# Optimization experiments

Hardware: AMD Instinct MI355X
Metric: run time of the kernel (lower is better)

## Reference

```python
import jax, jax.numpy as jnp
import numpy as np

T, B, IN, H, F, OUT = 2048, 32, 256, 512, 2048, 256


def setup_inputs() -> dict:
    key = jax.random.key(0)
    ks = jax.random.split(key, 9)
    s_in = 1.0 / np.sqrt(IN)
    s_h = 1.0 / np.sqrt(H)
    s_f = 1.0 / np.sqrt(F)
    return {
        "x": jax.random.normal(ks[0], (T, B, IN), dtype=jnp.float32),
        "Wg": jax.random.uniform(ks[1], (H, IN), jnp.float32, -s_in, s_in),
        "bg": jax.random.uniform(ks[2], (H,), jnp.float32, -s_in, s_in),
        "Wi": jax.random.uniform(ks[3], (H, IN), jnp.float32, -s_in, s_in),
        "bi": jax.random.uniform(ks[4], (H,), jnp.float32, -s_in, s_in),
        "W1": jax.random.uniform(ks[5], (F, H), jnp.float32, -s_h, s_h),
        "b1": jax.random.uniform(ks[6], (F,), jnp.float32, -s_h, s_h),
        "W2": jax.random.uniform(ks[7], (OUT, F), jnp.float32, -s_f, s_f),
        "b2": jax.random.uniform(ks[8], (OUT,), jnp.float32, -s_f, s_f),
    }


def _gilr_scan(a, b):
    # h_t = a_t * h_{t-1} + b_t with h_0 = 0  ->  parallel associative scan over time
    def combine(c1, c2):
        a1, b1 = c1
        a2, b2 = c2
        return (a1 * a2, b1 * a2 + b2)
    _, h = jax.lax.associative_scan(combine, (a, b), axis=0)
    return h


def reference(x, Wg, bg, Wi, bi, W1, b1, W2, b2):
    # x: (T, B, IN)
    g = jax.nn.sigmoid(jnp.einsum("tbi,hi->tbh", x, Wg) + bg)  # (T,B,H)
    i = jnp.tanh(jnp.einsum("tbi,hi->tbh", x, Wi) + bi)        # (T,B,H)
    h = _gilr_scan(g, (1.0 - g) * i)                             # (T,B,H)
    z = jax.nn.gelu(jnp.einsum("tbh,fh->tbf", h, W1) + b1, approximate=False)
    out = jnp.einsum("tbf,of->tbo", z, W2) + b2                  # (T,B,OUT)
    return out
```

## Files before the change

kernel.cpp:

```cpp
#include <hip/hip_runtime.h>
#include <hip/hip_fp16.h>
#include <math.h>


#define IN_DIM 256
#define H_DIM 512
#define F_DIM 2048
#define OUT_DIM 256

typedef _Float16 f16;
typedef _Float16 f16x8 __attribute__((ext_vector_type(8)));
typedef float f32x4 __attribute__((ext_vector_type(4)));

#define AS3(p) ((__attribute__((address_space(3))) void*)(p))
#define AS1(p) ((const __attribute__((address_space(1))) void*)(p))
#define MFMA16(d, x, y) d = __builtin_amdgcn_mfma_f32_16x16x32_f16(x, y, d, 0, 0, 0)


__global__ void cvt_kernel(const float* __restrict__ in, f16* __restrict__ out, int n8) {
  int i = blockIdx.x * blockDim.x + threadIdx.x;
  if (i >= n8) return;
  const float4* p = (const float4*)in + (size_t)i * 2;
  float4 a = p[0], b = p[1];
  f16x8 o = { (f16)a.x, (f16)a.y, (f16)a.z, (f16)a.w,
              (f16)b.x, (f16)b.y, (f16)b.z, (f16)b.w };
  *((f16x8*)out + i) = o;
}

__global__ void bias_cat_kernel(const float* __restrict__ bg, const float* __restrict__ bi,
                                float* __restrict__ bgi) {
  int t = threadIdx.x;
  bgi[t] = (t < 512) ? bg[t] : bi[t - 512];
}

__device__ __forceinline__ float sigmoid_fast(float v) {
  return __builtin_amdgcn_rcpf(1.0f + __expf(-v));
}
__device__ __forceinline__ float tanh_fast(float v) {
  return 1.0f - 2.0f * __builtin_amdgcn_rcpf(__expf(2.0f * v) + 1.0f);
}
__device__ __forceinline__ float gelu_fast(float v) {
  float u = v * v;
  float y = v * fmaf(0.0713548353f, u, 1.59576912161f);
  return v * __builtin_amdgcn_rcpf(1.0f + __expf(-y));
}


__global__ __launch_bounds__(256, 4) void gemm1_k(
    const f16* __restrict__ A, const f16* __restrict__ Bw,
    const float* __restrict__ bias, f16* __restrict__ Cout) {
  constexpr int LDA = 256, LDB = 256, LDC = 1024, NT = 8;
  __shared__ f16 lds[2][2][128][32];
  const int tid = threadIdx.x, wid = tid >> 6, lane = tid & 63;
  const int bid = blockIdx.x;
  const int m0 = ((bid & 7) * 64 + (bid >> 6)) * 128;
  const int n0 = ((bid >> 3) & 7) * 128;
  const int wr = (wid >> 1) * 64, wc = (wid & 1) * 64;

  const f16* srcA[2]; const f16* srcB[2];
#pragma unroll
  for (int q = 0; q < 2; ++q) {
    int s = (wid * 2 + q) * 64 + lane;
    int row = s >> 2, g = (s & 3) ^ ((row >> 1) & 3);
    srcA[q] = A + (size_t)(m0 + row) * LDA + g * 8;
    srcB[q] = Bw + (size_t)(n0 + row) * LDB + g * 8;
  }
  auto stage = [&](int buf, int kt) {
    f16* la = &lds[buf][0][0][0] + (wid * 2) * 512;
    f16* lb = &lds[buf][1][0][0] + (wid * 2) * 512;
#pragma unroll
    for (int q = 0; q < 2; ++q) {
      __builtin_amdgcn_global_load_lds(AS1(srcA[q] + kt * 32), AS3(la + q * 512), 16, 0, 0);
      __builtin_amdgcn_global_load_lds(AS1(srcB[q] + kt * 32), AS3(lb + q * 512), 16, 0, 0);
    }
  };
  const int r = lane & 15;
  const int cs = (((lane >> 4) ^ ((lane >> 1) & 3)) << 3);

  f32x4 acc[4][4] = {};
  stage(0, 0);
  for (int kt = 0; kt < NT; ++kt) {
    __syncthreads();
    if (kt + 1 < NT) stage((kt + 1) & 1, kt + 1);
    f16(*At)[32] = lds[kt & 1][0];
    f16(*Bt)[32] = lds[kt & 1][1];
    f16x8 af[4], bf[4];
#pragma unroll
    for (int i = 0; i < 4; ++i) af[i] = *(const f16x8*)&At[wr + i * 16 + r][cs];
#pragma unroll
    for (int i = 0; i < 4; ++i) bf[i] = *(const f16x8*)&Bt[wc + i * 16 + r][cs];
#pragma unroll
    for (int mi = 0; mi < 4; ++mi)
#pragma unroll
      for (int ni = 0; ni < 4; ++ni)
        MFMA16(acc[mi][ni], af[mi], bf[ni]);
  }

  __syncthreads();
  const bool sig = n0 < 512;
  f16* ep = &lds[0][0][0][0] + wid * 4096;
  const int rq = (lane >> 4) * 4;
#pragma unroll
  for (int ni = 0; ni < 4; ++ni) {
    float bv = bias[n0 + wc + ni * 16 + r];
    int cc = ni * 2 + (r >> 3);
#pragma unroll
    for (int mi = 0; mi < 4; ++mi) {
#pragma unroll
      for (int j = 0; j < 4; ++j) {
        int lrow = mi * 16 + rq + j;
        float v = acc[mi][ni][j] + bv;
        float av = sig ? sigmoid_fast(v) : tanh_fast(v);
        ep[lrow * 64 + ((cc ^ (lrow & 7)) << 3) + (r & 7)] = (f16)av;
      }
    }
  }
  asm volatile("s_waitcnt lgkmcnt(0)" ::: "memory");
  __builtin_amdgcn_sched_barrier(0);
#pragma unroll
  for (int t = 0; t < 8; ++t) {
    int idx = t * 64 + lane;
    int row = idx >> 3, c = idx & 7;
    f16x8 v = *(const f16x8*)(ep + row * 64 + ((c ^ (row & 7)) << 3));
    *(f16x8*)(Cout + (size_t)(m0 + wr + row) * LDC + n0 + wc + c * 8) = v;
  }
}


__global__ __launch_bounds__(256, 4) void gemm2_k(
    const f16* __restrict__ A, const f16* __restrict__ Bw,
    const float* __restrict__ bias, f16* __restrict__ Cout) {
  constexpr int LDA = 1024, LDB = 512, LDC = 2048, NT = 16;
  __shared__ f16 lds[2][2][128][32];
  const int tid = threadIdx.x, wid = tid >> 6, lane = tid & 63;
  const int bid = blockIdx.x;
  const int m0 = ((bid & 7) * 16 + (bid >> 7)) * 128;
  const int n0 = ((bid >> 3) & 15) * 128;
  const int wr = (wid >> 1) * 64, wc = (wid & 1) * 64;

  const f16* srcA[2]; const f16* srcB[2];
#pragma unroll
  for (int q = 0; q < 2; ++q) {
    int s = (wid * 2 + q) * 64 + lane;
    int row = s >> 2, g = (s & 3) ^ ((row >> 1) & 3);
    srcA[q] = A + (size_t)(m0 + row) * LDA + g * 8;
    srcB[q] = Bw + (size_t)(n0 + row) * LDB + g * 8;
  }
  auto stage = [&](int buf, int kt) {
    f16* la = &lds[buf][0][0][0] + (wid * 2) * 512;
    f16* lb = &lds[buf][1][0][0] + (wid * 2) * 512;
#pragma unroll
    for (int q = 0; q < 2; ++q) {
      __builtin_amdgcn_global_load_lds(AS1(srcA[q] + kt * 32), AS3(la + q * 512), 16, 0, 0);
      __builtin_amdgcn_global_load_lds(AS1(srcB[q] + kt * 32), AS3(lb + q * 512), 16, 0, 0);
    }
  };
  const int r = lane & 15;
  const int cs = (((lane >> 4) ^ ((lane >> 1) & 3)) << 3);

  f32x4 acc[4][4] = {};
  stage(0, 0);
  for (int kt = 0; kt < NT; ++kt) {
    __syncthreads();
    if (kt + 1 < NT) stage((kt + 1) & 1, kt + 1);
    f16(*At)[32] = lds[kt & 1][0];
    f16(*Bt)[32] = lds[kt & 1][1];
    f16x8 af[4], bf[4];
#pragma unroll
    for (int i = 0; i < 4; ++i) af[i] = *(const f16x8*)&At[wr + i * 16 + r][cs];
#pragma unroll
    for (int i = 0; i < 4; ++i) bf[i] = *(const f16x8*)&Bt[wc + i * 16 + r][cs];
#pragma unroll
    for (int mi = 0; mi < 4; ++mi)
#pragma unroll
      for (int ni = 0; ni < 4; ++ni)
        MFMA16(acc[mi][ni], af[mi], bf[ni]);
  }

  __syncthreads();
  f16* ep = &lds[0][0][0][0] + wid * 4096;
  const int rq = (lane >> 4) * 4;
#pragma unroll
  for (int ni = 0; ni < 4; ++ni) {
    float bv = bias[n0 + wc + ni * 16 + r];
    int cc = ni * 2 + (r >> 3);
#pragma unroll
    for (int mi = 0; mi < 4; ++mi) {
#pragma unroll
      for (int j = 0; j < 4; ++j) {
        int lrow = mi * 16 + rq + j;
        float v = gelu_fast(acc[mi][ni][j] + bv);
        ep[lrow * 64 + ((cc ^ (lrow & 7)) << 3) + (r & 7)] = (f16)v;
      }
    }
  }
  asm volatile("s_waitcnt lgkmcnt(0)" ::: "memory");
  __builtin_amdgcn_sched_barrier(0);
#pragma unroll
  for (int t = 0; t < 8; ++t) {
    int idx = t * 64 + lane;
    int row = idx >> 3, c = idx & 7;
    f16x8 v = *(const f16x8*)(ep + row * 64 + ((c ^ (row & 7)) << 3));
    *(f16x8*)(Cout + (size_t)(m0 + wr + row) * LDC + n0 + wc + c * 8) = v;
  }
}


__global__ __launch_bounds__(256, 2) void gemm3_k(
    const f16* __restrict__ A, const f16* __restrict__ Bw,
    const float* __restrict__ bias, float* __restrict__ Cout) {
  constexpr int LDA = 2048, LDB = 2048, LDC = 256, NT = 32;
  __shared__ f16 lds[2][2][128][64];
  const int tid = threadIdx.x, wid = tid >> 6, lane = tid & 63;
  const int bid = blockIdx.x;
  const int m0 = ((bid & 7) * 16 + (bid >> 4)) * 128;
  const int n0 = ((bid >> 3) & 1) * 128;
  const int wr = (wid >> 1) * 64, wc = (wid & 1) * 64;

  auto stage = [&](int buf, int kt) {
    const f16* ga = A + (size_t)m0 * LDA + kt * 64;
    const f16* gb = Bw + (size_t)n0 * LDB + kt * 64;
    f16* la = &lds[buf][0][0][0];
    f16* lb = &lds[buf][1][0][0];
#pragma unroll
    for (int q = 0; q < 4; ++q) {
      int seg = (wid << 2) + q;
      int s = seg * 64 + lane;
      int row = s >> 3, col = (s & 7) << 3;
      __builtin_amdgcn_global_load_lds(AS1(ga + (size_t)row * LDA + col),
                                       AS3(la + seg * 512), 16, 0, 0);
      __builtin_amdgcn_global_load_lds(AS1(gb + (size_t)row * LDB + col),
                                       AS3(lb + seg * 512), 16, 0, 0);
    }
  };

  f32x4 acc[4][4] = {};
  stage(0, 0);
  for (int kt = 0; kt < NT; ++kt) {
    __syncthreads();
    if (kt + 1 < NT) stage((kt + 1) & 1, kt + 1);
    f16(*At)[64] = lds[kt & 1][0];
    f16(*Bt)[64] = lds[kt & 1][1];
    const int r = lane & 15, cg = (lane >> 4) << 3;
#pragma unroll
    for (int kk = 0; kk < 2; ++kk) {
      f16x8 af[4], bf[4];
#pragma unroll
      for (int i = 0; i < 4; ++i)
        af[i] = *(const f16x8*)&At[wr + i * 16 + r][kk * 32 + cg];
#pragma unroll
      for (int i = 0; i < 4; ++i)
        bf[i] = *(const f16x8*)&Bt[wc + i * 16 + r][kk * 32 + cg];
#pragma unroll
      for (int mi = 0; mi < 4; ++mi)
#pragma unroll
        for (int ni = 0; ni < 4; ++ni)
          MFMA16(acc[mi][ni], af[mi], bf[ni]);
    }
  }
  const int r = lane & 15, rq = (lane >> 4) * 4;
#pragma unroll
  for (int ni = 0; ni < 4; ++ni) {
    int col = n0 + wc + ni * 16 + r;
    float bv = bias[col];
#pragma unroll
    for (int mi = 0; mi < 4; ++mi) {
#pragma unroll
      for (int j = 0; j < 4; ++j) {
        int row = m0 + wr + mi * 16 + rq + j;
        Cout[(size_t)row * LDC + col] = acc[mi][ni][j] + bv;
      }
    }
  }
}


#define NCH 16384
#define NCHUNK 32
#define CLEN 64

__global__ void scan_p1(const f16* __restrict__ ab, float* __restrict__ cA,
                        float* __restrict__ cH) {
  int ch = blockIdx.x * 256 + threadIdx.x;
  int c = blockIdx.y;
  const f16* pg = ab + (size_t)(c * CLEN) * 32768 + (ch >> 9) * 1024 + (ch & 511);
  const f16* pi = pg + 512;
  float A = 1.f, Hl = 0.f;
  for (int t = 0; t < CLEN; ++t) {
    float g = (float)pg[0];
    float ii = (float)pi[0];
    Hl = fmaf(g, Hl - ii, ii);
    A *= g;
    pg += 32768; pi += 32768;
  }
  cA[c * NCH + ch] = A;
  cH[c * NCH + ch] = Hl;
}

__global__ void scan_p2(const float* __restrict__ cA, const float* __restrict__ cH,
                        float* __restrict__ st) {
  int ch = blockIdx.x * 256 + threadIdx.x;
  float h0 = 0.f;
  for (int c = 0; c < NCHUNK; ++c) {
    st[c * NCH + ch] = h0;
    h0 = cA[c * NCH + ch] * h0 + cH[c * NCH + ch];
  }
}

__global__ void scan_p3(f16* __restrict__ ab, const float* __restrict__ st) {
  int ch = blockIdx.x * 256 + threadIdx.x;
  int c = blockIdx.y;
  f16* pg = ab + (size_t)(c * CLEN) * 32768 + (ch >> 9) * 1024 + (ch & 511);
  const f16* pi = pg + 512;
  float hv = st[c * NCH + ch];
  for (int t = 0; t < CLEN; ++t) {
    float g = (float)pg[0];
    float ii = (float)pi[0];
    hv = fmaf(g, hv - ii, ii);
    pg[0] = (f16)hv;
    pg += 32768; pi += 32768;
  }
}


extern "C" void kernel_launch(void* const* d_in, const int* in_sizes, int n_in,
                              void* d_out, int out_size, void* d_ws, size_t ws_size,
                              hipStream_t stream) {
  const float* x  = (const float*)d_in[0];
  const float* Wg = (const float*)d_in[1];
  const float* bg = (const float*)d_in[2];
  const float* Wi = (const float*)d_in[3];
  const float* bi = (const float*)d_in[4];
  const float* W1 = (const float*)d_in[5];
  const float* b1 = (const float*)d_in[6];
  const float* W2 = (const float*)d_in[7];
  const float* b2 = (const float*)d_in[8];
  float* out = (float*)d_out;

  char* ws = (char*)d_ws;
  f16*   wgi16 = (f16*)(ws + 0);
  f16*   w116  = (f16*)(ws + 524288);
  f16*   w216  = (f16*)(ws + 2621440);
  float* bgi   = (float*)(ws + 3670016);
  f16*   x16   = (f16*)(ws + 4194304);
  f16*   ab16  = (f16*)(ws + 37748736);
  float* cA    = (float*)(ws + 171966464);
  float* cH    = (float*)(ws + 174063616);
  float* st    = (float*)(ws + 176160768);
  f16*   z16   = (f16*)(ws + 178257920);
  if (ws_size < 245366784) return;

  cvt_kernel<<<64, 256, 0, stream>>>(Wg, wgi16, 16384);
  cvt_kernel<<<64, 256, 0, stream>>>(Wi, wgi16 + 131072, 16384);
  cvt_kernel<<<512, 256, 0, stream>>>(W1, w116, 131072);
  cvt_kernel<<<256, 256, 0, stream>>>(W2, w216, 65536);
  bias_cat_kernel<<<1, 1024, 0, stream>>>(bg, bi, bgi);
  cvt_kernel<<<8192, 256, 0, stream>>>(x, x16, 2097152);

  gemm1_k<<<4096, 256, 0, stream>>>(x16, wgi16, bgi, ab16);

  scan_p1<<<dim3(64, NCHUNK), 256, 0, stream>>>(ab16, cA, cH);
  scan_p2<<<64, 256, 0, stream>>>(cA, cH, st);
  scan_p3<<<dim3(64, NCHUNK), 256, 0, stream>>>(ab16, st);

  for (int s = 0; s < 4; ++s) {
    const f16* hs = ab16 + (size_t)s * 16384 * 1024;
    gemm2_k<<<2048, 256, 0, stream>>>(hs, w116, b1, z16);
    gemm3_k<<<256, 256, 0, stream>>>(z16, w216, b2, out + (size_t)s * 16384 * 256);
  }
}
```

Measured before the change: 516.7 us.

## Enlarge gemm2 tile to 256x128, fuse weight conversions, tweak launch bounds

gemm2 moves from 128x128 to 256x128 block tiles, so each wave computes a 128x64 sub-tile with 8x4 MFMA accumulators. This raises reuse of the B tile and halves the grid, at the cost of more registers and LDS per block. Two variants with different occupancy bounds (3 and 2 blocks) are used for different slices of the sequence. The four weight conversion launches are merged into one kernel, and gemm1 launch bounds are raised to 5.

```diff
diff --git a/kernel.cpp b/kernel.cpp
--- a/kernel.cpp
+++ b/kernel.cpp
@@ -27,6 +27,21 @@
   *((f16x8*)out + i) = o;
 }
 
+__global__ void cvt_w(const float* __restrict__ Wg, const float* __restrict__ Wi,
+                      const float* __restrict__ W1, const float* __restrict__ W2,
+                      f16* __restrict__ wgi, f16* __restrict__ w1, f16* __restrict__ w2) {
+  int i = blockIdx.x * 256 + threadIdx.x;
+  const float* src; f16* dst; int l;
+  if (i < 16384)       { l = i;          src = Wg + (size_t)l * 8; dst = wgi + (size_t)l * 8; }
+  else if (i < 32768)  { l = i - 16384;  src = Wi + (size_t)l * 8; dst = wgi + 131072 + (size_t)l * 8; }
+  else if (i < 163840) { l = i - 32768;  src = W1 + (size_t)l * 8; dst = w1 + (size_t)l * 8; }
+  else                 { l = i - 163840; src = W2 + (size_t)l * 8; dst = w2 + (size_t)l * 8; }
+  float4 a = ((const float4*)src)[0], b = ((const float4*)src)[1];
+  f16x8 o = { (f16)a.x, (f16)a.y, (f16)a.z, (f16)a.w,
+              (f16)b.x, (f16)b.y, (f16)b.z, (f16)b.w };
+  *(f16x8*)dst = o;
+}
+
 __global__ void bias_cat_kernel(const float* __restrict__ bg, const float* __restrict__ bi,
                                 float* __restrict__ bgi) {
   int t = threadIdx.x;
@@ -46,7 +61,7 @@
 }
 
 
-__global__ __launch_bounds__(256, 4) void gemm1_k(
+__global__ __launch_bounds__(256, 5) void gemm1_k(
     const f16* __restrict__ A, const f16* __restrict__ Bw,
     const float* __restrict__ bias, f16* __restrict__ Cout) {
   constexpr int LDA = 256, LDB = 256, LDC = 1024, NT = 8;
@@ -127,83 +142,102 @@
 }
 
 
-__global__ __launch_bounds__(256, 4) void gemm2_k(
+#define GEMM2_BODY                                                                       \
+  constexpr int LDA = 1024, LDB = 512, LDC = 2048, NT = 16;                              \
+  __shared__ f16 lds[24576];                                                             \
+  const int tid = threadIdx.x, wid = tid >> 6, lane = tid & 63;                          \
+  const int lr = lane & 15;                                                              \
+  const int bid = blockIdx.x;                                                            \
+  const int m0 = ((bid & 7) * 8 + (bid >> 7)) * 256;                                     \
+  const int n0 = ((bid >> 3) & 15) * 128;                                                \
+  const int wr = (wid >> 1) * 128, wc = (wid & 1) * 64;                                  \
+  const f16* srcA[4];                                                                    \
+  const f16* srcB[2];                                                                    \
+  _Pragma("unroll")                                                                      \
+  for (int q = 0; q < 4; ++q) {                                                          \
+    int s = wid * 256 + q * 64 + lane;                                                   \
+    int row = s >> 2, g = (s & 3) ^ ((row >> 1) & 3);                                    \
+    srcA[q] = A + (size_t)(m0 + row) * LDA + g * 8;                                      \
+  }                                                                                      \
+  _Pragma("unroll")                                                                      \
+  for (int q = 0; q < 2; ++q) {                                                          \
+    int s = wid * 128 + q * 64 + lane;                                                   \
+    int row = s >> 2, g = (s & 3) ^ ((row >> 1) & 3);                                    \
+    srcB[q] = Bw + (size_t)(n0 + row) * LDB + g * 8;                                     \
+  }                                                                                      \
+  auto stage = [&](int buf, int kt) {                                                    \
+    _Pragma("unroll")                                                                    \
+    for (int q = 0; q < 4; ++q)                                                          \
+      __builtin_amdgcn_global_load_lds(AS1(srcA[q] + kt * 32),                           \
+          AS3(lds + buf * 8192 + wid * 2048 + q * 512), 16, 0, 0);                       \
+    _Pragma("unroll")                                                                    \
+    for (int q = 0; q < 2; ++q)                                                          \
+      __builtin_amdgcn_global_load_lds(AS1(srcB[q] + kt * 32),                           \
+          AS3(lds + 16384 + buf * 4096 + wid * 1024 + q * 512), 16, 0, 0);               \
+  };                                                                                     \
+  const int qsf = (((lane >> 4) ^ ((lr >> 1) & 3)) << 3);                                \
+  f32x4 acc[8][4] = {};                                                                  \
+  stage(0, 0);                                                                           \
+  for (int kt = 0; kt < NT; ++kt) {                                                      \
+    const int cur = kt & 1;                                                              \
+    __syncthreads();                                                                     \
+    if (kt + 1 < NT) stage(cur ^ 1, kt + 1);                                             \
+    f16x8 af[8], bf[4];                                                                  \
+    _Pragma("unroll")                                                                    \
+    for (int mi = 0; mi < 8; ++mi)                                                       \
+      af[mi] = *(const f16x8*)(lds + cur * 8192 + (wr + mi * 16 + lr) * 32 + qsf);       \
+    _Pragma("unroll")                                                                    \
+    for (int ni = 0; ni < 4; ++ni)                                                       \
+      bf[ni] = *(const f16x8*)(lds + 16384 + cur * 4096 + (wc + ni * 16 + lr) * 32 + qsf); \
+    _Pragma("unroll")                                                                    \
+    for (int mi = 0; mi < 8; ++mi)                                                       \
+      _Pragma("unroll")                                                                  \
+      for (int ni = 0; ni < 4; ++ni)                                                     \
+        MFMA16(acc[mi][ni], af[mi], bf[ni]);                                             \
+  }                                                                                      \
+  __syncthreads();                                                                       \
+  f16* ep = lds + wid * 4096;                                                            \
+  const int rq = (lane >> 4) * 4;                                                        \
+  _Pragma("unroll")                                                                      \
+  for (int h = 0; h < 2; ++h) {                                                          \
+    _Pragma("unroll")                                                                    \
+    for (int mi = 0; mi < 4; ++mi) {                                                     \
+      _Pragma("unroll")                                                                  \
+      for (int ni = 0; ni < 4; ++ni) {                                                   \
+        float bv = bias[n0 + wc + ni * 16 + lr];                                         \
+        int cc = ni * 2 + (lr >> 3);                                                     \
+        _Pragma("unroll")                                                                \
+        for (int j = 0; j < 4; ++j) {                                                    \
+          int lrow = mi * 16 + rq + j;                                                   \
+          float v = gelu_fast(acc[h * 4 + mi][ni][j] + bv);                              \
+          ep[lrow * 64 + ((cc ^ (lrow & 7)) << 3) + (lr & 7)] = (f16)v;                  \
+        }                                                                                \
+      }                                                                                  \
+    }                                                                                    \
+    asm volatile("s_waitcnt lgkmcnt(0)" ::: "memory");                                   \
+    __builtin_amdgcn_sched_barrier(0);                                                   \
+    _Pragma("unroll")                                                                    \
+    for (int t = 0; t < 8; ++t) {                                                        \
+      int idx = t * 64 + lane;                                                           \
+      int row = idx >> 3, c = idx & 7;                                                   \
+      f16x8 v = *(const f16x8*)(ep + row * 64 + ((c ^ (row & 7)) << 3));                 \
+      *(f16x8*)(Cout + (size_t)(m0 + wr + h * 64 + row) * LDC + n0 + wc + c * 8) = v;    \
+    }                                                                                    \
+    asm volatile("s_waitcnt lgkmcnt(0)" ::: "memory");                                   \
+    __builtin_amdgcn_sched_barrier(0);                                                   \
+  }
+
+__global__ __launch_bounds__(256, 3) void gemm2_k3(
     const f16* __restrict__ A, const f16* __restrict__ Bw,
     const float* __restrict__ bias, f16* __restrict__ Cout) {
-  constexpr int LDA = 1024, LDB = 512, LDC = 2048, NT = 16;
-  __shared__ f16 lds[2][2][128][32];
-  const int tid = threadIdx.x, wid = tid >> 6, lane = tid & 63;
-  const int bid = blockIdx.x;
-  const int m0 = ((bid & 7) * 16 + (bid >> 7)) * 128;
-  const int n0 = ((bid >> 3) & 15) * 128;
-  const int wr = (wid >> 1) * 64, wc = (wid & 1) * 64;
-
-  const f16* srcA[2]; const f16* srcB[2];
-#pragma unroll
-  for (int q = 0; q < 2; ++q) {
-    int s = (wid * 2 + q) * 64 + lane;
-    int row = s >> 2, g = (s & 3) ^ ((row >> 1) & 3);
-    srcA[q] = A + (size_t)(m0 + row) * LDA + g * 8;
-    srcB[q] = Bw + (size_t)(n0 + row) * LDB + g * 8;
-  }
-  auto stage = [&](int buf, int kt) {
-    f16* la = &lds[buf][0][0][0] + (wid * 2) * 512;
-    f16* lb = &lds[buf][1][0][0] + (wid * 2) * 512;
-#pragma unroll
-    for (int q = 0; q < 2; ++q) {
-      __builtin_amdgcn_global_load_lds(AS1(srcA[q] + kt * 32), AS3(la + q * 512), 16, 0, 0);
-      __builtin_amdgcn_global_load_lds(AS1(srcB[q] + kt * 32), AS3(lb + q * 512), 16, 0, 0);
-    }
-  };
-  const int r = lane & 15;
-  const int cs = (((lane >> 4) ^ ((lane >> 1) & 3)) << 3);
-
-  f32x4 acc[4][4] = {};
-  stage(0, 0);
-  for (int kt = 0; kt < NT; ++kt) {
-    __syncthreads();
-    if (kt + 1 < NT) stage((kt + 1) & 1, kt + 1);
-    f16(*At)[32] = lds[kt & 1][0];
-    f16(*Bt)[32] = lds[kt & 1][1];
-    f16x8 af[4], bf[4];
-#pragma unroll
-    for (int i = 0; i < 4; ++i) af[i] = *(const f16x8*)&At[wr + i * 16 + r][cs];
-#pragma unroll
-    for (int i = 0; i < 4; ++i) bf[i] = *(const f16x8*)&Bt[wc + i * 16 + r][cs];
-#pragma unroll
-    for (int mi = 0; mi < 4; ++mi)
-#pragma unroll
-      for (int ni = 0; ni < 4; ++ni)
-        MFMA16(acc[mi][ni], af[mi], bf[ni]);
-  }
-
-  __syncthreads();
-  f16* ep = &lds[0][0][0][0] + wid * 4096;
-  const int rq = (lane >> 4) * 4;
-#pragma unroll
-  for (int ni = 0; ni < 4; ++ni) {
-    float bv = bias[n0 + wc + ni * 16 + r];
-    int cc = ni * 2 + (r >> 3);
-#pragma unroll
-    for (int mi = 0; mi < 4; ++mi) {
-#pragma unroll
-      for (int j = 0; j < 4; ++j) {
-        int lrow = mi * 16 + rq + j;
-        float v = gelu_fast(acc[mi][ni][j] + bv);
-        ep[lrow * 64 + ((cc ^ (lrow & 7)) << 3) + (r & 7)] = (f16)v;
-      }
-    }
-  }
-  asm volatile("s_waitcnt lgkmcnt(0)" ::: "memory");
-  __builtin_amdgcn_sched_barrier(0);
-#pragma unroll
-  for (int t = 0; t < 8; ++t) {
-    int idx = t * 64 + lane;
-    int row = idx >> 3, c = idx & 7;
-    f16x8 v = *(const f16x8*)(ep + row * 64 + ((c ^ (row & 7)) << 3));
-    *(f16x8*)(Cout + (size_t)(m0 + wr + row) * LDC + n0 + wc + c * 8) = v;
-  }
-}
+  GEMM2_BODY
+}
+__global__ __launch_bounds__(256, 2) void gemm2_k2(
+    const f16* __restrict__ A, const f16* __restrict__ Bw,
+    const float* __restrict__ bias, f16* __restrict__ Cout) {
+  GEMM2_BODY
+}
+#undef GEMM2_BODY
 
 
 __global__ __launch_bounds__(256, 2) void gemm3_k(
@@ -350,10 +384,7 @@
   f16*   z16   = (f16*)(ws + 178257920);
   if (ws_size < 245366784) return;
 
-  cvt_kernel<<<64, 256, 0, stream>>>(Wg, wgi16, 16384);
-  cvt_kernel<<<64, 256, 0, stream>>>(Wi, wgi16 + 131072, 16384);
-  cvt_kernel<<<512, 256, 0, stream>>>(W1, w116, 131072);
-  cvt_kernel<<<256, 256, 0, stream>>>(W2, w216, 65536);
+  cvt_w<<<896, 256, 0, stream>>>(Wg, Wi, W1, W2, wgi16, w116, w216);
   bias_cat_kernel<<<1, 1024, 0, stream>>>(bg, bi, bgi);
   cvt_kernel<<<8192, 256, 0, stream>>>(x, x16, 2097152);
 
@@ -365,7 +396,10 @@
 
   for (int s = 0; s < 4; ++s) {
     const f16* hs = ab16 + (size_t)s * 16384 * 1024;
-    gemm2_k<<<2048, 256, 0, stream>>>(hs, w116, b1, z16);
+    if (s < 2)
+      gemm2_k3<<<1024, 256, 0, stream>>>(hs, w116, b1, z16);
+    else
+      gemm2_k2<<<1024, 256, 0, stream>>>(hs, w116, b1, z16);
     gemm3_k<<<256, 256, 0, stream>>>(z16, w216, b2, out + (size_t)s * 16384 * 256);
   }
 }
```

After: 520.0 us. About the same (+0.7%).
